# Kernel tuning notes

Hardware: AMD Instinct MI355X
Metric: run time of the kernel (lower is better)

The kernel has to match this reference:

```python
import jax, jax.numpy as jnp
import numpy as np

N_NODES = 100000

def gcn_conv(x, W, b, src, dst, n_nodes):
    # PyG GCNConv: out = D^{-1/2} (A + I) D^{-1/2} (x W) + b, deg includes self-loop
    h = x @ W  # [N, H]
    ones = jnp.ones(src.shape[0], dtype=x.dtype)
    deg = jax.ops.segment_sum(ones, dst, num_segments=n_nodes) + 1.0  # +1 self-loop
    dinv = jax.lax.rsqrt(deg)  # deg >= 1, no zeros
    norm = dinv[src] * dinv[dst]  # [E]
    msg = h[src] * norm[:, None]  # [E, H] gather + scale
    agg = jax.ops.segment_sum(msg, dst, num_segments=n_nodes)  # scatter-add
    self_contrib = h * (dinv * dinv)[:, None]  # self-loop term norm = dinv_i^2
    return agg + self_contrib + b


def setup_inputs() -> dict:
    key = jax.random.key(0)
    ks = jax.random.split(key, 6)
    F_IN, H, E = 128, 128, 1600000
    x = jax.random.normal(ks[0], (N_NODES, F_IN), dtype=jnp.float32)
    edge_index = jax.random.randint(ks[1], (2, E), 0, N_NODES, dtype=jnp.int32)
    s = 1.0 / np.sqrt(F_IN)
    W1 = jax.random.normal(ks[2], (F_IN, H), dtype=jnp.float32) * s
    b1 = jnp.zeros((H,), dtype=jnp.float32)
    W2 = jax.random.normal(ks[3], (H, H), dtype=jnp.float32) * (1.0 / np.sqrt(H))
    b2 = jnp.zeros((H,), dtype=jnp.float32)
    Wlin = jax.random.normal(ks[4], (H, 1), dtype=jnp.float32) * (1.0 / np.sqrt(H))
    blin = jnp.zeros((1,), dtype=jnp.float32)
    return {"x": x, "edge_index": edge_index, "W1": W1, "b1": b1,
            "W2": W2, "b2": b2, "Wlin": Wlin, "blin": blin}


def reference(x, edge_index, W1, b1, W2, b2, Wlin, blin):
    src, dst = edge_index[0], edge_index[1]
    h = gcn_conv(x, W1, b1, src, dst, N_NODES)
    h = jax.nn.relu(h)
    h = gcn_conv(h, W2, b2, src, dst, N_NODES)
    h = jax.nn.relu(h)
    out = h @ Wlin + blin  # [N, 1]
    return out.squeeze(-1)  # [N]
```

## Files before the change

### kernel.cpp

```cpp
#include <hip/hip_runtime.h>
#include <hip/hip_fp16.h>

#define NFEAT 128

typedef _Float16 v8hf __attribute__((ext_vector_type(8)));
typedef _Float16 v4hf __attribute__((ext_vector_type(4)));
typedef float v4f __attribute__((ext_vector_type(4)));

__global__ void k_deg_rank_w(const int* __restrict__ dst, int* __restrict__ deg,
                             int* __restrict__ rank, int E, int N,
                             const float* __restrict__ W1, const float* __restrict__ W2,
                             _Float16* __restrict__ Wt1, _Float16* __restrict__ Wt2) {
  int e = blockIdx.x * blockDim.x + threadIdx.x;
  if (e < E) rank[e] = atomicAdd(&deg[dst[e]], 1);
  else if (e < E + N) rank[e] = atomicAdd(&deg[e - E], 1);
  else if (e < E + N + 32768) {
    int idx = e - E - N;
    const float* W = (idx < 16384) ? W1 : W2;
    _Float16* Wt = (idx < 16384) ? Wt1 : Wt2;
    int i = idx & 16383;
    int k = i >> 7, n = i & 127;
    Wt[n * 128 + k] = (_Float16)W[k * 128 + n];
  }
}

__device__ __forceinline__ int wave_incl_scan(int v, int lane) {
  #pragma unroll
  for (int off = 1; off < 64; off <<= 1) {
    int t = __shfl_up(v, off, 64);
    if (lane >= off) v += t;
  }
  return v;
}

__global__ __launch_bounds__(256) void k_scan_blocks(const int* __restrict__ deg,
    int* __restrict__ base, int* __restrict__ partials,
    float* __restrict__ dinv, int n) {
  __shared__ int lds[4];
  const int tid = threadIdx.x;
  const int lane = tid & 63;
  const int wv = tid >> 6;
  int i0 = (blockIdx.x << 9) + (tid << 1);
  int a = (i0 < n) ? deg[i0] : 0;
  int b = (i0 + 1 < n) ? deg[i0 + 1] : 0;
  if (i0 < n) dinv[i0] = rsqrtf((float)a);
  if (i0 + 1 < n) dinv[i0 + 1] = rsqrtf((float)b);
  int inc = wave_incl_scan(a + b, lane);
  if (lane == 63) lds[wv] = inc;
  __syncthreads();
  int woff = 0, tot = 0;
  #pragma unroll
  for (int w = 0; w < 4; w++) {
    int t = lds[w];
    tot += t;
    if (w < wv) woff += t;
  }
  int ex = woff + inc - (a + b);
  const int N1 = n + 1;
  if (i0 < N1) base[i0] = ex;
  if (i0 + 1 < N1) base[i0 + 1] = ex + a;
  if (tid == 255) partials[blockIdx.x] = tot;
}

__global__ __launch_bounds__(256) void k_scan_partials(int* __restrict__ partials,
                                                       int nb) {
  __shared__ int lds[4];
  const int tid = threadIdx.x;
  const int lane = tid & 63;
  const int wv = tid >> 6;
  int v = (tid < nb) ? partials[tid] : 0;
  int inc = wave_incl_scan(v, lane);
  if (lane == 63) lds[wv] = inc;
  __syncthreads();
  int woff = 0;
  #pragma unroll
  for (int w = 0; w < 4; w++) if (w < wv) woff += lds[w];
  if (tid < nb) partials[tid] = woff + inc - v;
}

template <typename AT>
__device__ __forceinline__ void gemm_tile(
    const AT* __restrict__ A, const _Float16* __restrict__ Wt,
    const float* __restrict__ dinv, _Float16* __restrict__ g16, int N, int tile,
    _Float16 (*As)[136], _Float16 (*Ws)[136]) {
  const int tid = threadIdx.x;
  const int row0 = tile * 64;

  if constexpr (sizeof(AT) == 4) {
    #pragma unroll
    for (int i = 0; i < 8; i++) {
      int idx = tid + i * 256;
      int row = idx >> 5;
      int c4 = idx & 31;
      int gr = row0 + row; gr = (gr < N) ? gr : (N - 1);
      float4 v = *(const float4*)((const float*)A + (size_t)gr * NFEAT + c4 * 4);
      v4hf h;
      h[0] = (_Float16)v.x; h[1] = (_Float16)v.y;
      h[2] = (_Float16)v.z; h[3] = (_Float16)v.w;
      *(v4hf*)&As[row][c4 * 4] = h;
    }
  } else {
    #pragma unroll
    for (int i = 0; i < 4; i++) {
      int idx = tid + i * 256;
      int row = idx >> 4;
      int c8 = idx & 15;
      int gr = row0 + row; gr = (gr < N) ? gr : (N - 1);
      *(uint4*)&As[row][c8 * 8] =
          *(const uint4*)((const _Float16*)A + (size_t)gr * NFEAT + c8 * 8);
    }
  }
  #pragma unroll
  for (int i = 0; i < 8; i++) {
    int idx = tid + i * 256;
    int row = idx >> 4;
    int c8 = idx & 15;
    *(uint4*)&Ws[row][c8 * 8] = *(const uint4*)(Wt + (size_t)row * 128 + c8 * 8);
  }
  __syncthreads();

  const int wv = tid >> 6;
  const int lane = tid & 63;
  const int m = lane & 15;
  const int q = lane >> 4;

  v4f acc[8] = {};
  const _Float16* arow = &As[wv * 16 + m][0];
  #pragma unroll
  for (int kt = 0; kt < 4; kt++) {
    v8hf af = *(const v8hf*)(arow + kt * 32 + q * 8);
    #pragma unroll
    for (int ct = 0; ct < 8; ct++) {
      v8hf bf = *(const v8hf*)(&Ws[ct * 16 + m][kt * 32 + q * 8]);
      acc[ct] = __builtin_amdgcn_mfma_f32_16x16x32_f16(af, bf, acc[ct], 0, 0, 0);
    }
  }

  float dv[4];
  #pragma unroll
  for (int r = 0; r < 4; r++) {
    int nd = row0 + wv * 16 + q * 4 + r;
    int c = (nd < N) ? nd : (N - 1);
    dv[r] = dinv[c];
  }

  __syncthreads();
  #pragma unroll
  for (int ct = 0; ct < 8; ct++)
    #pragma unroll
    for (int r = 0; r < 4; r++)
      As[wv * 16 + q * 4 + r][ct * 16 + m] = (_Float16)(acc[ct][r] * dv[r]);
  __syncthreads();

  #pragma unroll
  for (int i = 0; i < 4; i++) {
    int idx = tid + i * 256;
    int row = idx >> 4;
    int c8 = idx & 15;
    int gr = row0 + row;
    if (gr < N)
      *(v8hf*)(g16 + (size_t)gr * NFEAT + c8 * 8) = *(const v8hf*)&As[row][c8 * 8];
  }
}

__global__ __launch_bounds__(256) void k_sg1(
    const int* __restrict__ src, const int* __restrict__ dst,
    const int* __restrict__ rank, const int* __restrict__ base,
    const int* __restrict__ partials, int* __restrict__ ssrc,
    const float* __restrict__ x, const _Float16* __restrict__ Wt1,
    const float* __restrict__ dinv, _Float16* __restrict__ g16,
    int E, int N, int gg) {
  __shared__ _Float16 As[64][136];
  __shared__ _Float16 Ws[128][136];
  int id = blockIdx.x;
  if (id < 2 * gg && (id & 1)) {
    int tile = id >> 1;
    if (tile == 0 && threadIdx.x < 16) {
      v8hf z;
      #pragma unroll
      for (int j = 0; j < 8; j++) z[j] = (_Float16)0.f;
      *(v8hf*)(g16 + (size_t)N * NFEAT + threadIdx.x * 8) = z;
    }
    gemm_tile<float>(x, Wt1, dinv, g16, N, tile, As, Ws);
    return;
  }
  id = (id < 2 * gg) ? (id >> 1) : (id - gg);
  int e = id * 256 + threadIdx.x;
  if (e < E) {
    int d = dst[e];
    ssrc[base[d] + partials[d >> 9] + rank[e]] = src[e];
  } else if (e < E + N) {
    int nn = e - E;
    ssrc[base[nn] + partials[nn >> 9] + rank[e]] = nn;
  }
}

__global__ __launch_bounds__(256) void k_gemm2(
    const _Float16* __restrict__ A, const _Float16* __restrict__ Wt,
    const float* __restrict__ dinv, _Float16* __restrict__ g16, int N) {
  __shared__ _Float16 As[64][136];
  __shared__ _Float16 Ws[128][136];
  gemm_tile<_Float16>(A, Wt, dinv, g16, N, blockIdx.x, As, Ws);
}

__global__ __launch_bounds__(256) void k_agg(
    const _Float16* __restrict__ g, const float* __restrict__ dinv,
    const int* __restrict__ base, const int* __restrict__ partials,
    const int* __restrict__ ssrc,
    const float* __restrict__ bias, _Float16* __restrict__ hB, int N) {
  const int lane = threadIdx.x & 63;
  const int n = blockIdx.x * 4 + (threadIdx.x >> 6);
  if (n >= N) return;
  const int gq = lane >> 4;
  const int l = lane & 15;
  const int b0 = base[n] + partials[n >> 9];
  const int b1 = base[n + 1] + partials[(n + 1) >> 9];

  int e = b0;
  int p0 = e + gq, p1 = e + 4 + gq;
  int i0 = ssrc[p0], i1 = ssrc[p1];
  i0 = (p0 < b1) ? i0 : N;
  i1 = (p1 < b1) ? i1 : N;
  v8hf r0 = *(const v8hf*)(g + (size_t)i0 * NFEAT + l * 8);
  v8hf r1 = *(const v8hf*)(g + (size_t)i1 * NFEAT + l * 8);
  int e2 = e + 8;
  int j0 = N, j1 = N;
  if (e2 < b1) {
    int q0 = e2 + gq, q1 = e2 + 4 + gq;
    j0 = ssrc[q0]; j1 = ssrc[q1];
    j0 = (q0 < b1) ? j0 : N;
    j1 = (q1 < b1) ? j1 : N;
  }

  float acc[8] = {};
  while (true) {
    bool more = (e2 < b1);
    v8hf s0, s1;
    if (more) {
      s0 = *(const v8hf*)(g + (size_t)j0 * NFEAT + l * 8);
      s1 = *(const v8hf*)(g + (size_t)j1 * NFEAT + l * 8);
    }
    int e3 = e2 + 8;
    int c0 = N, c1 = N;
    if (e3 < b1) {
      int q0 = e3 + gq, q1 = e3 + 4 + gq;
      c0 = ssrc[q0]; c1 = ssrc[q1];
      c0 = (q0 < b1) ? c0 : N;
      c1 = (q1 < b1) ? c1 : N;
    }
    #pragma unroll
    for (int j = 0; j < 8; j++) acc[j] += (float)r0[j] + (float)r1[j];
    if (!more) break;
    r0 = s0; r1 = s1;
    j0 = c0; j1 = c1;
    e2 = e3;
  }

  #pragma unroll
  for (int j = 0; j < 8; j++) {
    acc[j] += __shfl_xor(acc[j], 16, 64);
    acc[j] += __shfl_xor(acc[j], 32, 64);
  }
  if (gq == 0) {
    float dvn = dinv[n];
    const float* bp = bias + l * 8;
    float4 bb0 = *(const float4*)(bp);
    float4 bb1 = *(const float4*)(bp + 4);
    float bv[8] = {bb0.x, bb0.y, bb0.z, bb0.w, bb1.x, bb1.y, bb1.z, bb1.w};
    v8hf o;
    #pragma unroll
    for (int j = 0; j < 8; j++)
      o[j] = (_Float16)fmaxf(acc[j] * dvn + bv[j], 0.f);
    *(v8hf*)(hB + (size_t)n * NFEAT + l * 8) = o;
  }
}

__global__ __launch_bounds__(256) void k_agg_final(
    const _Float16* __restrict__ g, const float* __restrict__ dinv,
    const int* __restrict__ base, const int* __restrict__ partials,
    const int* __restrict__ ssrc,
    const float* __restrict__ bias, const float* __restrict__ wlin,
    const float* __restrict__ blin, float* __restrict__ out, int N) {
  const int lane = threadIdx.x & 63;
  const int n = blockIdx.x * 4 + (threadIdx.x >> 6);
  if (n >= N) return;
  const int gq = lane >> 4;
  const int l = lane & 15;
  const int b0 = base[n] + partials[n >> 9];
  const int b1 = base[n + 1] + partials[(n + 1) >> 9];

  int e = b0;
  int p0 = e + gq, p1 = e + 4 + gq;
  int i0 = ssrc[p0], i1 = ssrc[p1];
  i0 = (p0 < b1) ? i0 : N;
  i1 = (p1 < b1) ? i1 : N;
  v8hf r0 = *(const v8hf*)(g + (size_t)i0 * NFEAT + l * 8);
  v8hf r1 = *(const v8hf*)(g + (size_t)i1 * NFEAT + l * 8);
  int e2 = e + 8;
  int j0 = N, j1 = N;
  if (e2 < b1) {
    int q0 = e2 + gq, q1 = e2 + 4 + gq;
    j0 = ssrc[q0]; j1 = ssrc[q1];
    j0 = (q0 < b1) ? j0 : N;
    j1 = (q1 < b1) ? j1 : N;
  }

  float acc[8] = {};
  while (true) {
    bool more = (e2 < b1);
    v8hf s0, s1;
    if (more) {
      s0 = *(const v8hf*)(g + (size_t)j0 * NFEAT + l * 8);
      s1 = *(const v8hf*)(g + (size_t)j1 * NFEAT + l * 8);
    }
    int e3 = e2 + 8;
    int c0 = N, c1 = N;
    if (e3 < b1) {
      int q0 = e3 + gq, q1 = e3 + 4 + gq;
      c0 = ssrc[q0]; c1 = ssrc[q1];
      c0 = (q0 < b1) ? c0 : N;
      c1 = (q1 < b1) ? c1 : N;
    }
    #pragma unroll
    for (int j = 0; j < 8; j++) acc[j] += (float)r0[j] + (float)r1[j];
    if (!more) break;
    r0 = s0; r1 = s1;
    j0 = c0; j1 = c1;
    e2 = e3;
  }

  #pragma unroll
  for (int j = 0; j < 8; j++) {
    acc[j] += __shfl_xor(acc[j], 16, 64);
    acc[j] += __shfl_xor(acc[j], 32, 64);
  }
  float dvn = dinv[n];
  const float* bp = bias + l * 8;
  const float* wp = wlin + l * 8;
  float4 bb0 = *(const float4*)(bp);
  float4 bb1 = *(const float4*)(bp + 4);
  float4 wl0 = *(const float4*)(wp);
  float4 wl1 = *(const float4*)(wp + 4);
  float bv[8] = {bb0.x, bb0.y, bb0.z, bb0.w, bb1.x, bb1.y, bb1.z, bb1.w};
  float wv[8] = {wl0.x, wl0.y, wl0.z, wl0.w, wl1.x, wl1.y, wl1.z, wl1.w};
  float pv = 0.f;
  #pragma unroll
  for (int j = 0; j < 8; j++)
    pv += fmaxf(acc[j] * dvn + bv[j], 0.f) * wv[j];
  pv += __shfl_xor(pv, 1, 64);
  pv += __shfl_xor(pv, 2, 64);
  pv += __shfl_xor(pv, 4, 64);
  pv += __shfl_xor(pv, 8, 64);
  if (lane == 0) out[n] = pv + blin[0];
}

extern "C" void kernel_launch(void* const* d_in, const int* in_sizes, int n_in,
                              void* d_out, int out_size, void* d_ws, size_t ws_size,
                              hipStream_t stream) {
  const float* x    = (const float*)d_in[0];
  const int*   ei   = (const int*)d_in[1];
  const float* W1   = (const float*)d_in[2];
  const float* b1   = (const float*)d_in[3];
  const float* W2   = (const float*)d_in[4];
  const float* b2   = (const float*)d_in[5];
  const float* Wlin = (const float*)d_in[6];
  const float* blin = (const float*)d_in[7];
  const int N = in_sizes[0] / NFEAT;
  const int E = in_sizes[1] / 2;
  const int* src = ei;
  const int* dst = ei + E;
  const int Etot = E + N;

  int* ws_i = (int*)d_ws;
  size_t off = 0;
  int* deg      = ws_i + off; off += N;
  int* base     = ws_i + off; off += (size_t)N + 1;
  off = (off + 3) & ~(size_t)3;
  int* partials = ws_i + off; off += 256;
  int* ssrc     = ws_i + off; off += Etot + 8;
  float* dinv   = (float*)(ws_i + off); off += N;
  off = (off + 3) & ~(size_t)3;
  _Float16* Wt1 = (_Float16*)(ws_i + off); off += 8192;
  _Float16* Wt2 = (_Float16*)(ws_i + off); off += 8192;
  _Float16* g16 = (_Float16*)(ws_i + off); off += (size_t)(N + 1) * 64;
  _Float16* hB  = (_Float16*)(ws_i + off); off += (size_t)N * 64;
  int* rank = (int*)hB;

  hipMemsetAsync(deg, 0, (size_t)N * sizeof(int), stream);

  const int tpbE = 256;
  const int gE = (Etot + 32768 + tpbE - 1) / tpbE;
  k_deg_rank_w<<<gE, tpbE, 0, stream>>>(dst, deg, rank, E, N, W1, W2, Wt1, Wt2);

  const int nb = (N + 1 + 511) / 512;
  k_scan_blocks<<<nb, 256, 0, stream>>>(deg, base, partials, dinv, N);
  k_scan_partials<<<1, 256, 0, stream>>>(partials, nb);

  const int gg = (N + 63) / 64;
  const int ga = (N + 3) / 4;
  const int scb = (Etot + 255) / 256;
  k_sg1<<<scb + gg, 256, 0, stream>>>(src, dst, rank, base, partials, ssrc,
                                      x, Wt1, dinv, g16, E, N, gg);
  k_agg<<<ga, 256, 0, stream>>>(g16, dinv, base, partials, ssrc, b1, hB, N);
  k_gemm2<<<gg, 256, 0, stream>>>(hB, Wt2, dinv, g16, N);
  k_agg_final<<<ga, 256, 0, stream>>>(g16, dinv, base, partials, ssrc, b2,
                                      Wlin, blin, (float*)d_out, N);
}
```

Measured before the change: 376.3 us.

## Fuse layer-1 aggregation with layer-2 GEMM into one kernel

The first-layer aggregation now writes its ReLU'd fp16 rows for 16 nodes into shared memory, and the same block immediately multiplies them by W2 with MFMA and scales by dinv. This removes the hB round trip through global memory and one kernel launch. Two separate g buffers (gA, gB) are used so the second-layer input does not overwrite the first, and rank now aliases gB. Each block handles 4 nodes per wave sequentially, so there is less parallelism per node, and Wt2 is read straight from global memory per block.

```diff
diff --git a/kernel.cpp b/kernel.cpp
--- a/kernel.cpp
+++ b/kernel.cpp
@@ -168,20 +168,21 @@
     const int* __restrict__ rank, const int* __restrict__ base,
     const int* __restrict__ partials, int* __restrict__ ssrc,
     const float* __restrict__ x, const _Float16* __restrict__ Wt1,
-    const float* __restrict__ dinv, _Float16* __restrict__ g16,
-    int E, int N, int gg) {
+    const float* __restrict__ dinv, _Float16* __restrict__ gA,
+    _Float16* __restrict__ gB, int E, int N, int gg) {
   __shared__ _Float16 As[64][136];
   __shared__ _Float16 Ws[128][136];
   int id = blockIdx.x;
   if (id < 2 * gg && (id & 1)) {
     int tile = id >> 1;
-    if (tile == 0 && threadIdx.x < 16) {
+    if (tile == 0 && threadIdx.x < 32) {
       v8hf z;
       #pragma unroll
       for (int j = 0; j < 8; j++) z[j] = (_Float16)0.f;
-      *(v8hf*)(g16 + (size_t)N * NFEAT + threadIdx.x * 8) = z;
-    }
-    gemm_tile<float>(x, Wt1, dinv, g16, N, tile, As, Ws);
+      _Float16* p = (threadIdx.x < 16) ? gA : gB;
+      *(v8hf*)(p + (size_t)N * NFEAT + (threadIdx.x & 15) * 8) = z;
+    }
+    gemm_tile<float>(x, Wt1, dinv, gA, N, tile, As, Ws);
     return;
   }
   id = (id < 2 * gg) ? (id >> 1) : (id - gg);
@@ -195,84 +196,117 @@
   }
 }
 
-__global__ __launch_bounds__(256) void k_gemm2(
-    const _Float16* __restrict__ A, const _Float16* __restrict__ Wt,
-    const float* __restrict__ dinv, _Float16* __restrict__ g16, int N) {
-  __shared__ _Float16 As[64][136];
-  __shared__ _Float16 Ws[128][136];
-  gemm_tile<_Float16>(A, Wt, dinv, g16, N, blockIdx.x, As, Ws);
-}
-
-__global__ __launch_bounds__(256) void k_agg(
+__global__ __launch_bounds__(256) void k_agg_g2(
     const _Float16* __restrict__ g, const float* __restrict__ dinv,
     const int* __restrict__ base, const int* __restrict__ partials,
-    const int* __restrict__ ssrc,
-    const float* __restrict__ bias, _Float16* __restrict__ hB, int N) {
-  const int lane = threadIdx.x & 63;
-  const int n = blockIdx.x * 4 + (threadIdx.x >> 6);
-  if (n >= N) return;
+    const int* __restrict__ ssrc, const float* __restrict__ bias,
+    const _Float16* __restrict__ Wt2, _Float16* __restrict__ gB, int N) {
+  __shared__ _Float16 As[16][136];
+  const int tid = threadIdx.x;
+  const int lane = tid & 63;
+  const int wv = tid >> 6;
   const int gq = lane >> 4;
   const int l = lane & 15;
-  const int b0 = base[n] + partials[n >> 9];
-  const int b1 = base[n + 1] + partials[(n + 1) >> 9];
-
-  int e = b0;
-  int p0 = e + gq, p1 = e + 4 + gq;
-  int i0 = ssrc[p0], i1 = ssrc[p1];
-  i0 = (p0 < b1) ? i0 : N;
-  i1 = (p1 < b1) ? i1 : N;
-  v8hf r0 = *(const v8hf*)(g + (size_t)i0 * NFEAT + l * 8);
-  v8hf r1 = *(const v8hf*)(g + (size_t)i1 * NFEAT + l * 8);
-  int e2 = e + 8;
-  int j0 = N, j1 = N;
-  if (e2 < b1) {
-    int q0 = e2 + gq, q1 = e2 + 4 + gq;
-    j0 = ssrc[q0]; j1 = ssrc[q1];
-    j0 = (q0 < b1) ? j0 : N;
-    j1 = (q1 < b1) ? j1 : N;
-  }
-
-  float acc[8] = {};
-  while (true) {
-    bool more = (e2 < b1);
-    v8hf s0, s1;
-    if (more) {
-      s0 = *(const v8hf*)(g + (size_t)j0 * NFEAT + l * 8);
-      s1 = *(const v8hf*)(g + (size_t)j1 * NFEAT + l * 8);
-    }
-    int e3 = e2 + 8;
-    int c0 = N, c1 = N;
-    if (e3 < b1) {
-      int q0 = e3 + gq, q1 = e3 + 4 + gq;
-      c0 = ssrc[q0]; c1 = ssrc[q1];
-      c0 = (q0 < b1) ? c0 : N;
-      c1 = (q1 < b1) ? c1 : N;
-    }
-    #pragma unroll
-    for (int j = 0; j < 8; j++) acc[j] += (float)r0[j] + (float)r1[j];
-    if (!more) break;
-    r0 = s0; r1 = s1;
-    j0 = c0; j1 = c1;
-    e2 = e3;
-  }
-
-  #pragma unroll
-  for (int j = 0; j < 8; j++) {
-    acc[j] += __shfl_xor(acc[j], 16, 64);
-    acc[j] += __shfl_xor(acc[j], 32, 64);
-  }
-  if (gq == 0) {
-    float dvn = dinv[n];
-    const float* bp = bias + l * 8;
-    float4 bb0 = *(const float4*)(bp);
-    float4 bb1 = *(const float4*)(bp + 4);
-    float bv[8] = {bb0.x, bb0.y, bb0.z, bb0.w, bb1.x, bb1.y, bb1.z, bb1.w};
-    v8hf o;
-    #pragma unroll
-    for (int j = 0; j < 8; j++)
-      o[j] = (_Float16)fmaxf(acc[j] * dvn + bv[j], 0.f);
-    *(v8hf*)(hB + (size_t)n * NFEAT + l * 8) = o;
-  }
+  const int n0 = blockIdx.x * 16;
+
+  #pragma unroll 1
+  for (int s = 0; s < 4; s++) {
+    const int n = n0 + wv * 4 + s;
+    if (n < N) {
+      const int b0 = base[n] + partials[n >> 9];
+      const int b1 = base[n + 1] + partials[(n + 1) >> 9];
+
+      int e = b0;
+      int p0 = e + gq, p1 = e + 4 + gq;
+      int i0 = ssrc[p0], i1 = ssrc[p1];
+      i0 = (p0 < b1) ? i0 : N;
+      i1 = (p1 < b1) ? i1 : N;
+      v8hf r0 = *(const v8hf*)(g + (size_t)i0 * NFEAT + l * 8);
+      v8hf r1 = *(const v8hf*)(g + (size_t)i1 * NFEAT + l * 8);
+      int e2 = e + 8;
+      int j0 = N, j1 = N;
+      if (e2 < b1) {
+        int q0 = e2 + gq, q1 = e2 + 4 + gq;
+        j0 = ssrc[q0]; j1 = ssrc[q1];
+        j0 = (q0 < b1) ? j0 : N;
+        j1 = (q1 < b1) ? j1 : N;
+      }
+
+      float acc[8] = {};
+      while (true) {
+        bool more = (e2 < b1);
+        v8hf s0, s1;
+        if (more) {
+          s0 = *(const v8hf*)(g + (size_t)j0 * NFEAT + l * 8);
+          s1 = *(const v8hf*)(g + (size_t)j1 * NFEAT + l * 8);
+        }
+        int e3 = e2 + 8;
+        int c0 = N, c1 = N;
+        if (e3 < b1) {
+          int q0 = e3 + gq, q1 = e3 + 4 + gq;
+          c0 = ssrc[q0]; c1 = ssrc[q1];
+          c0 = (q0 < b1) ? c0 : N;
+          c1 = (q1 < b1) ? c1 : N;
+        }
+        #pragma unroll
+        for (int j = 0; j < 8; j++) acc[j] += (float)r0[j] + (float)r1[j];
+        if (!more) break;
+        r0 = s0; r1 = s1;
+        j0 = c0; j1 = c1;
+        e2 = e3;
+      }
+
+      #pragma unroll
+      for (int j = 0; j < 8; j++) {
+        acc[j] += __shfl_xor(acc[j], 16, 64);
+        acc[j] += __shfl_xor(acc[j], 32, 64);
+      }
+      if (gq == 0) {
+        float dvn = dinv[n];
+        const float* bp = bias + l * 8;
+        float4 bb0 = *(const float4*)(bp);
+        float4 bb1 = *(const float4*)(bp + 4);
+        float bv[8] = {bb0.x, bb0.y, bb0.z, bb0.w, bb1.x, bb1.y, bb1.z, bb1.w};
+        v8hf o;
+        #pragma unroll
+        for (int j = 0; j < 8; j++)
+          o[j] = (_Float16)fmaxf(acc[j] * dvn + bv[j], 0.f);
+        *(v8hf*)&As[wv * 4 + s][l * 8] = o;
+      }
+    }
+  }
+  __syncthreads();
+
+  v4f acc2[2] = {};
+  #pragma unroll
+  for (int kt = 0; kt < 4; kt++) {
+    v8hf af = *(const v8hf*)(&As[l][kt * 32 + gq * 8]);
+    #pragma unroll
+    for (int c = 0; c < 2; c++) {
+      int ct = wv * 2 + c;
+      v8hf bf = *(const v8hf*)(Wt2 + (size_t)(ct * 16 + l) * 128 + kt * 32 + gq * 8);
+      acc2[c] = __builtin_amdgcn_mfma_f32_16x16x32_f16(af, bf, acc2[c], 0, 0, 0);
+    }
+  }
+  float dv[4];
+  #pragma unroll
+  for (int r = 0; r < 4; r++) {
+    int nd = n0 + gq * 4 + r;
+    int c = (nd < N) ? nd : (N - 1);
+    dv[r] = dinv[c];
+  }
+  __syncthreads();
+  #pragma unroll
+  for (int c = 0; c < 2; c++)
+    #pragma unroll
+    for (int r = 0; r < 4; r++)
+      As[gq * 4 + r][(wv * 2 + c) * 16 + l] = (_Float16)(acc2[c][r] * dv[r]);
+  __syncthreads();
+
+  int row = tid >> 4, c8 = tid & 15;
+  int gr = n0 + row;
+  if (gr < N)
+    *(v8hf*)(gB + (size_t)gr * NFEAT + c8 * 8) = *(const v8hf*)&As[row][c8 * 8];
 }
 
 __global__ __launch_bounds__(256) void k_agg_final(
@@ -382,9 +416,9 @@
   off = (off + 3) & ~(size_t)3;
   _Float16* Wt1 = (_Float16*)(ws_i + off); off += 8192;
   _Float16* Wt2 = (_Float16*)(ws_i + off); off += 8192;
-  _Float16* g16 = (_Float16*)(ws_i + off); off += (size_t)(N + 1) * 64;
-  _Float16* hB  = (_Float16*)(ws_i + off); off += (size_t)N * 64;
-  int* rank = (int*)hB;
+  _Float16* gA  = (_Float16*)(ws_i + off); off += (size_t)(N + 1) * 64;
+  _Float16* gB  = (_Float16*)(ws_i + off); off += (size_t)(N + 1) * 64;
+  int* rank = (int*)gB;
 
   hipMemsetAsync(deg, 0, (size_t)N * sizeof(int), stream);
 
@@ -397,12 +431,13 @@
   k_scan_partials<<<1, 256, 0, stream>>>(partials, nb);
 
   const int gg = (N + 63) / 64;
-  const int ga = (N + 3) / 4;
   const int scb = (Etot + 255) / 256;
   k_sg1<<<scb + gg, 256, 0, stream>>>(src, dst, rank, base, partials, ssrc,
-                                      x, Wt1, dinv, g16, E, N, gg);
-  k_agg<<<ga, 256, 0, stream>>>(g16, dinv, base, partials, ssrc, b1, hB, N);
-  k_gemm2<<<gg, 256, 0, stream>>>(hB, Wt2, dinv, g16, N);
-  k_agg_final<<<ga, 256, 0, stream>>>(g16, dinv, base, partials, ssrc, b2,
+                                      x, Wt1, dinv, gA, gB, E, N, gg);
+  const int ga16 = (N + 15) / 16;
+  k_agg_g2<<<ga16, 256, 0, stream>>>(gA, dinv, base, partials, ssrc, b1,
+                                     Wt2, gB, N);
+  const int ga = (N + 3) / 4;
+  k_agg_final<<<ga, 256, 0, stream>>>(gB, dinv, base, partials, ssrc, b2,
                                       Wlin, blin, (float*)d_out, N);
 }
```

After: 374.8 us. About the same (-0.4%).

## Split feature dimension across two blocks per node in aggregation kernels

Applied to the files above, without the earlier changes.

Each node's aggregation is now split into two 64-feature halves handled by paired blocks, so each wavefront covers 16 edges per step (8 slots of 8 lanes) instead of 8 edges across full rows. This doubles the number of blocks and the edges in flight per wave, aimed at hiding gather latency on high-degree nodes. The final projection now combines the two halves with atomicAdd into a zeroed output, which adds a memset and atomics. Each gathered row segment shrinks to 128 bytes, and the ssrc index list is read twice per node.

```diff
diff --git a/kernel.cpp b/kernel.cpp
--- a/kernel.cpp
+++ b/kernel.cpp
@@ -209,24 +209,26 @@
     const int* __restrict__ ssrc,
     const float* __restrict__ bias, _Float16* __restrict__ hB, int N) {
   const int lane = threadIdx.x & 63;
-  const int n = blockIdx.x * 4 + (threadIdx.x >> 6);
+  const int chunk = blockIdx.x & 1;
+  const int n = (blockIdx.x >> 1) * 4 + (threadIdx.x >> 6);
   if (n >= N) return;
-  const int gq = lane >> 4;
-  const int l = lane & 15;
+  const int slot = lane >> 3;
+  const int l = lane & 7;
   const int b0 = base[n] + partials[n >> 9];
   const int b1 = base[n + 1] + partials[(n + 1) >> 9];
+  const _Float16* gc = g + chunk * 64;
 
   int e = b0;
-  int p0 = e + gq, p1 = e + 4 + gq;
+  int p0 = e + slot, p1 = e + 8 + slot;
   int i0 = ssrc[p0], i1 = ssrc[p1];
   i0 = (p0 < b1) ? i0 : N;
   i1 = (p1 < b1) ? i1 : N;
-  v8hf r0 = *(const v8hf*)(g + (size_t)i0 * NFEAT + l * 8);
-  v8hf r1 = *(const v8hf*)(g + (size_t)i1 * NFEAT + l * 8);
-  int e2 = e + 8;
+  v8hf r0 = *(const v8hf*)(gc + (size_t)i0 * NFEAT + l * 8);
+  v8hf r1 = *(const v8hf*)(gc + (size_t)i1 * NFEAT + l * 8);
+  int e2 = e + 16;
   int j0 = N, j1 = N;
   if (e2 < b1) {
-    int q0 = e2 + gq, q1 = e2 + 4 + gq;
+    int q0 = e2 + slot, q1 = e2 + 8 + slot;
     j0 = ssrc[q0]; j1 = ssrc[q1];
     j0 = (q0 < b1) ? j0 : N;
     j1 = (q1 < b1) ? j1 : N;
@@ -237,13 +239,13 @@
     bool more = (e2 < b1);
     v8hf s0, s1;
     if (more) {
-      s0 = *(const v8hf*)(g + (size_t)j0 * NFEAT + l * 8);
-      s1 = *(const v8hf*)(g + (size_t)j1 * NFEAT + l * 8);
-    }
-    int e3 = e2 + 8;
+      s0 = *(const v8hf*)(gc + (size_t)j0 * NFEAT + l * 8);
+      s1 = *(const v8hf*)(gc + (size_t)j1 * NFEAT + l * 8);
+    }
+    int e3 = e2 + 16;
     int c0 = N, c1 = N;
     if (e3 < b1) {
-      int q0 = e3 + gq, q1 = e3 + 4 + gq;
+      int q0 = e3 + slot, q1 = e3 + 8 + slot;
       c0 = ssrc[q0]; c1 = ssrc[q1];
       c0 = (q0 < b1) ? c0 : N;
       c1 = (q1 < b1) ? c1 : N;
@@ -258,12 +260,13 @@
 
   #pragma unroll
   for (int j = 0; j < 8; j++) {
+    acc[j] += __shfl_xor(acc[j], 8, 64);
     acc[j] += __shfl_xor(acc[j], 16, 64);
     acc[j] += __shfl_xor(acc[j], 32, 64);
   }
-  if (gq == 0) {
+  if (slot == 0) {
     float dvn = dinv[n];
-    const float* bp = bias + l * 8;
+    const float* bp = bias + chunk * 64 + l * 8;
     float4 bb0 = *(const float4*)(bp);
     float4 bb1 = *(const float4*)(bp + 4);
     float bv[8] = {bb0.x, bb0.y, bb0.z, bb0.w, bb1.x, bb1.y, bb1.z, bb1.w};
@@ -271,7 +274,7 @@
     #pragma unroll
     for (int j = 0; j < 8; j++)
       o[j] = (_Float16)fmaxf(acc[j] * dvn + bv[j], 0.f);
-    *(v8hf*)(hB + (size_t)n * NFEAT + l * 8) = o;
+    *(v8hf*)(hB + (size_t)n * NFEAT + chunk * 64 + l * 8) = o;
   }
 }
 
@@ -282,24 +285,26 @@
     const float* __restrict__ bias, const float* __restrict__ wlin,
     const float* __restrict__ blin, float* __restrict__ out, int N) {
   const int lane = threadIdx.x & 63;
-  const int n = blockIdx.x * 4 + (threadIdx.x >> 6);
+  const int chunk = blockIdx.x & 1;
+  const int n = (blockIdx.x >> 1) * 4 + (threadIdx.x >> 6);
   if (n >= N) return;
-  const int gq = lane >> 4;
-  const int l = lane & 15;
+  const int slot = lane >> 3;
+  const int l = lane & 7;
   const int b0 = base[n] + partials[n >> 9];
   const int b1 = base[n + 1] + partials[(n + 1) >> 9];
+  const _Float16* gc = g + chunk * 64;
 
   int e = b0;
-  int p0 = e + gq, p1 = e + 4 + gq;
+  int p0 = e + slot, p1 = e + 8 + slot;
   int i0 = ssrc[p0], i1 = ssrc[p1];
   i0 = (p0 < b1) ? i0 : N;
   i1 = (p1 < b1) ? i1 : N;
-  v8hf r0 = *(const v8hf*)(g + (size_t)i0 * NFEAT + l * 8);
-  v8hf r1 = *(const v8hf*)(g + (size_t)i1 * NFEAT + l * 8);
-  int e2 = e + 8;
+  v8hf r0 = *(const v8hf*)(gc + (size_t)i0 * NFEAT + l * 8);
+  v8hf r1 = *(const v8hf*)(gc + (size_t)i1 * NFEAT + l * 8);
+  int e2 = e + 16;
   int j0 = N, j1 = N;
   if (e2 < b1) {
-    int q0 = e2 + gq, q1 = e2 + 4 + gq;
+    int q0 = e2 + slot, q1 = e2 + 8 + slot;
     j0 = ssrc[q0]; j1 = ssrc[q1];
     j0 = (q0 < b1) ? j0 : N;
     j1 = (q1 < b1) ? j1 : N;
@@ -310,13 +315,13 @@
     bool more = (e2 < b1);
     v8hf s0, s1;
     if (more) {
-      s0 = *(const v8hf*)(g + (size_t)j0 * NFEAT + l * 8);
-      s1 = *(const v8hf*)(g + (size_t)j1 * NFEAT + l * 8);
-    }
-    int e3 = e2 + 8;
+      s0 = *(const v8hf*)(gc + (size_t)j0 * NFEAT + l * 8);
+      s1 = *(const v8hf*)(gc + (size_t)j1 * NFEAT + l * 8);
+    }
+    int e3 = e2 + 16;
     int c0 = N, c1 = N;
     if (e3 < b1) {
-      int q0 = e3 + gq, q1 = e3 + 4 + gq;
+      int q0 = e3 + slot, q1 = e3 + 8 + slot;
       c0 = ssrc[q0]; c1 = ssrc[q1];
       c0 = (q0 < b1) ? c0 : N;
       c1 = (q1 < b1) ? c1 : N;
@@ -331,12 +336,13 @@
 
   #pragma unroll
   for (int j = 0; j < 8; j++) {
+    acc[j] += __shfl_xor(acc[j], 8, 64);
     acc[j] += __shfl_xor(acc[j], 16, 64);
     acc[j] += __shfl_xor(acc[j], 32, 64);
   }
   float dvn = dinv[n];
-  const float* bp = bias + l * 8;
-  const float* wp = wlin + l * 8;
+  const float* bp = bias + chunk * 64 + l * 8;
+  const float* wp = wlin + chunk * 64 + l * 8;
   float4 bb0 = *(const float4*)(bp);
   float4 bb1 = *(const float4*)(bp + 4);
   float4 wl0 = *(const float4*)(wp);
@@ -350,8 +356,10 @@
   pv += __shfl_xor(pv, 1, 64);
   pv += __shfl_xor(pv, 2, 64);
   pv += __shfl_xor(pv, 4, 64);
-  pv += __shfl_xor(pv, 8, 64);
-  if (lane == 0) out[n] = pv + blin[0];
+  if (lane == 0) {
+    if (chunk == 0) pv += blin[0];
+    atomicAdd(out + n, pv);
+  }
 }
 
 extern "C" void kernel_launch(void* const* d_in, const int* in_sizes, int n_in,
@@ -377,7 +385,7 @@
   int* base     = ws_i + off; off += (size_t)N + 1;
   off = (off + 3) & ~(size_t)3;
   int* partials = ws_i + off; off += 256;
-  int* ssrc     = ws_i + off; off += Etot + 8;
+  int* ssrc     = ws_i + off; off += Etot + 16;
   float* dinv   = (float*)(ws_i + off); off += N;
   off = (off + 3) & ~(size_t)3;
   _Float16* Wt1 = (_Float16*)(ws_i + off); off += 8192;
@@ -387,6 +395,7 @@
   int* rank = (int*)hB;
 
   hipMemsetAsync(deg, 0, (size_t)N * sizeof(int), stream);
+  hipMemsetAsync(d_out, 0, (size_t)N * sizeof(float), stream);
 
   const int tpbE = 256;
   const int gE = (Etot + 32768 + tpbE - 1) / tpbE;
@@ -397,10 +406,10 @@
   k_scan_partials<<<1, 256, 0, stream>>>(partials, nb);
 
   const int gg = (N + 63) / 64;
-  const int ga = (N + 3) / 4;
   const int scb = (Etot + 255) / 256;
   k_sg1<<<scb + gg, 256, 0, stream>>>(src, dst, rank, base, partials, ssrc,
                                       x, Wt1, dinv, g16, E, N, gg);
+  const int ga = 2 * ((N + 3) / 4);
   k_agg<<<ga, 256, 0, stream>>>(g16, dinv, base, partials, ssrc, b1, hB, N);
   k_gemm2<<<gg, 256, 0, stream>>>(hB, Wt2, dinv, g16, N);
   k_agg_final<<<ga, 256, 0, stream>>>(g16, dinv, base, partials, ssrc, b2,
```

After: 442.8 us. 17.7% more time.
